# Performance work log

Hardware: AMD Instinct MI355X
Metric: run time of the kernel (lower is better)

Reference implementation:

```python
import jax, jax.numpy as jnp
import numpy as np

B, S, D = 2, 2048, 2048
H = 16
HD = D // H  # 128


def setup_inputs() -> dict:
    key = jax.random.key(0)
    k1, k2, k3 = jax.random.split(key, 3)
    scale = 0.02
    return {
        "hidden_states": jax.random.normal(k1, (B, S, D), dtype=jnp.float32),
        "c_attn_w": jax.random.normal(k2, (D, 3 * D), dtype=jnp.float32) * scale,
        "c_attn_b": jnp.zeros((3 * D,), dtype=jnp.float32),
        "c_proj_w": jax.random.normal(k3, (D, D), dtype=jnp.float32) * scale,
        "c_proj_b": jnp.zeros((D,), dtype=jnp.float32),
    }


def reference(hidden_states, c_attn_w, c_attn_b, c_proj_w, c_proj_b):
    # Conv1D: x @ W + b  (W is [in, out])
    qkv = hidden_states @ c_attn_w + c_attn_b            # [B,S,3D]
    q, k, v = jnp.split(qkv, 3, axis=-1)                 # each [B,S,D]

    def split_heads(t):
        return t.reshape(B, S, H, HD).transpose(0, 2, 1, 3)  # [B,H,S,HD]

    q, k, v = split_heads(q), split_heads(k), split_heads(v)

    # scaled dot-product scores (scale_attn_weights=True)
    scores = jnp.einsum("bhqd,bhkd->bhqk", q, k) / jnp.sqrt(
        jnp.asarray(HD, dtype=q.dtype)
    )
    # causal mask (tril bias buffer)
    causal = jnp.tril(jnp.ones((S, S), dtype=bool))
    mask_value = jnp.finfo(scores.dtype).min
    scores = jnp.where(causal[None, None, :, :], scores, mask_value)

    attn = jax.nn.softmax(scores, axis=-1)               # [B,H,S,S]
    ctx = jnp.einsum("bhqk,bhkd->bhqd", attn, v)         # [B,H,S,HD]
    ctx = ctx.transpose(0, 2, 1, 3).reshape(B, S, D)      # merge heads

    out = ctx @ c_proj_w + c_proj_b                       # [B,S,D]
    return out
```

## Files before the change

kernel.cpp:

```cpp
#include <hip/hip_runtime.h>

typedef unsigned short u16;
typedef __bf16 bfx8 __attribute__((ext_vector_type(8)));
typedef float f32x4 __attribute__((ext_vector_type(4)));

#define B_ 2
#define S_ 2048
#define D_ 2048
#define H_ 16
#define HD_ 128
#define SD_ 6144

__device__ __forceinline__ u16 f2bf(float f) {
  union { float f; unsigned u; } v; v.f = f;
  unsigned r = v.u + 0x7fffu + ((v.u >> 16) & 1u);
  return (u16)(r >> 16);
}
__device__ __forceinline__ float bf2f(u16 b) {
  union { unsigned u; float f; } v; v.u = ((unsigned)b) << 16;
  return v.f;
}
__device__ __forceinline__ void gload_lds16(const void* g, void* l) {
  __builtin_amdgcn_global_load_lds((const __attribute__((address_space(1))) void*)g,
                                   (__attribute__((address_space(3))) void*)l, 16, 0, 0);
}

#define BAR() do { asm volatile("" ::: "memory"); __builtin_amdgcn_s_barrier(); \
                   asm volatile("" ::: "memory"); } while (0)
#define WAIT_VM4() asm volatile("s_waitcnt vmcnt(4)" ::: "memory")
#define WAIT_VM3() asm volatile("s_waitcnt vmcnt(3)" ::: "memory")
#define WAIT_VM0() asm volatile("s_waitcnt vmcnt(0)" ::: "memory")

__device__ __forceinline__ void tile_coords(int BM, int BN, int& m0, int& n0) {
  int flat = blockIdx.x + gridDim.x * blockIdx.y;
  int xcd = flat & 7, li = flat >> 3;
  int MW = gridDim.y >> 3;
  int half = li >> 1, nn = li & 1;
  int mloc = half % MW, nw = half / MW;
  m0 = (xcd * MW + mloc) * BM;
  n0 = (nw * 2 + nn) * BN;
}

__global__ __launch_bounds__(256) void cvt_kernel(const float* __restrict__ in,
                                                  u16* __restrict__ out, int n4) {
  int i = blockIdx.x * blockDim.x + threadIdx.x;
  int stride = gridDim.x * blockDim.x;
  for (int idx = i; idx < n4; idx += stride) {
    float4 v = ((const float4*)in)[idx];
    uint2 o;
    o.x = (unsigned)f2bf(v.x) | ((unsigned)f2bf(v.y) << 16);
    o.y = (unsigned)f2bf(v.z) | ((unsigned)f2bf(v.w) << 16);
    ((uint2*)out)[idx] = o;
  }
}

__global__ __launch_bounds__(256) void transpose_cvt(const float* __restrict__ in,
                                                     u16* __restrict__ out,
                                                     int R, int C) {
  __shared__ float tile[32][33];
  int tx = threadIdx.x, ty = threadIdx.y;
  int c0 = blockIdx.x * 32, r0 = blockIdx.y * 32;
  for (int i = 0; i < 4; ++i)
    tile[ty + i * 8][tx] = in[(size_t)(r0 + ty + i * 8) * C + c0 + tx];
  __syncthreads();
  for (int i = 0; i < 4; ++i)
    out[(size_t)(c0 + ty + i * 8) * R + r0 + tx] = f2bf(tile[tx][ty + i * 8]);
}

__global__ __launch_bounds__(256) void transpose_v(const u16* __restrict__ qkv,
                                                   u16* __restrict__ vt) {
  __shared__ u16 tile[32][33];
  int tx = threadIdx.x, ty = threadIdx.y;
  int bh = blockIdx.z;
  int b = bh >> 4, h = bh & 15;
  int s0 = blockIdx.x * 32, d0 = blockIdx.y * 32;
  const u16* src = qkv + (size_t)b * S_ * SD_ + 2 * D_ + h * HD_;
  for (int i = 0; i < 4; ++i)
    tile[ty + i * 8][tx] = src[(size_t)(s0 + ty + i * 8) * SD_ + d0 + tx];
  __syncthreads();
  u16* dst = vt + (size_t)bh * HD_ * S_;
  for (int i = 0; i < 4; ++i)
    dst[(size_t)(d0 + ty + i * 8) * S_ + s0 + tx] = tile[tx][ty + i * 8];
}

template<int OUT_BF16>
__global__ __launch_bounds__(512, 2) void gemm8p(const u16* __restrict__ A,
                                                 const u16* __restrict__ Bt,
                                                 const float* __restrict__ bias,
                                                 void* __restrict__ Cout,
                                                 int M, int N, int K) {
  __shared__ u16 lds[2][2][2][256 * 32];

  int t = threadIdx.x, l = t & 63, w = t >> 6;
  int lr = l & 15, lg = l >> 4;
  int wr = w >> 2, wc = w & 3;

  int m0, n0;
  tile_coords(256, 256, m0, n0);

  f32x4 acc[8][4];
#pragma unroll
  for (int i = 0; i < 8; ++i)
#pragma unroll
    for (int j = 0; j < 4; ++j)
#pragma unroll
      for (int r = 0; r < 4; ++r) acc[i][j][r] = 0.0f;

  int srow = t >> 2, sc = t & 3;
  const u16* As0 = A  + (size_t)(m0 + srow) * K + ((sc ^ ((srow >> 1) & 3)) * 8);
  const u16* Bs0 = Bt + (size_t)(n0 + srow) * K + ((sc ^ ((srow >> 1) & 3)) * 8);
  size_t hstep = (size_t)128 * K;

#define STG_A(BUF, KH, KOFF) do { \
    gload_lds16(As0 + (KOFF),         &lds[0][BUF][KH][t * 8]); \
    gload_lds16(As0 + hstep + (KOFF), &lds[0][BUF][KH][4096 + t * 8]); \
  } while (0)
#define STG_B(BUF, KH, KOFF) do { \
    gload_lds16(Bs0 + (KOFF),         &lds[1][BUF][KH][t * 8]); \
    gload_lds16(Bs0 + hstep + (KOFF), &lds[1][BUF][KH][4096 + t * 8]); \
  } while (0)

  int NT = K >> 6;
  int rsw = (lg ^ ((lr >> 1) & 3)) * 8;
  int arow = wr * 128 + lr;
  int brow = wc * 64 + lr;

  STG_A(0, 0, 0); STG_B(0, 0, 0); STG_A(0, 1, 32); STG_B(0, 1, 32);
  WAIT_VM4();
  BAR();

  for (int g = 0; g < NT; ++g) {
    int cb = g & 1, sb = cb ^ 1;
    int koff = (g + 1) * 64;
    bool stg = (g + 1 < NT);
    bfx8 a0[4], a1[4], bfr[4];

    if (stg) { STG_A(sb, 0, koff); STG_B(sb, 0, koff); }
#pragma unroll
    for (int i = 0; i < 4; ++i) {
      a0[i] = *(const bfx8*)&lds[0][cb][0][(arow + i * 16) * 32 + rsw];
      a1[i] = *(const bfx8*)&lds[0][cb][0][(arow + 64 + i * 16) * 32 + rsw];
    }
#pragma unroll
    for (int j = 0; j < 4; ++j)
      bfr[j] = *(const bfx8*)&lds[1][cb][0][(brow + j * 16) * 32 + rsw];
    __builtin_amdgcn_s_setprio(1);
#pragma unroll
    for (int i = 0; i < 4; ++i)
#pragma unroll
      for (int j = 0; j < 4; ++j) {
        acc[i][j]     = __builtin_amdgcn_mfma_f32_16x16x32_bf16(a0[i], bfr[j], acc[i][j], 0, 0, 0);
        acc[4 + i][j] = __builtin_amdgcn_mfma_f32_16x16x32_bf16(a1[i], bfr[j], acc[4 + i][j], 0, 0, 0);
      }
    __builtin_amdgcn_s_setprio(0);
    if (stg) WAIT_VM4(); else WAIT_VM0();
    BAR();

    if (stg) { STG_A(sb, 1, koff + 32); STG_B(sb, 1, koff + 32); }
#pragma unroll
    for (int i = 0; i < 4; ++i) {
      a0[i] = *(const bfx8*)&lds[0][cb][1][(arow + i * 16) * 32 + rsw];
      a1[i] = *(const bfx8*)&lds[0][cb][1][(arow + 64 + i * 16) * 32 + rsw];
    }
#pragma unroll
    for (int j = 0; j < 4; ++j)
      bfr[j] = *(const bfx8*)&lds[1][cb][1][(brow + j * 16) * 32 + rsw];
    __builtin_amdgcn_s_setprio(1);
#pragma unroll
    for (int i = 0; i < 4; ++i)
#pragma unroll
      for (int j = 0; j < 4; ++j) {
        acc[i][j]     = __builtin_amdgcn_mfma_f32_16x16x32_bf16(a0[i], bfr[j], acc[i][j], 0, 0, 0);
        acc[4 + i][j] = __builtin_amdgcn_mfma_f32_16x16x32_bf16(a1[i], bfr[j], acc[4 + i][j], 0, 0, 0);
      }
    __builtin_amdgcn_s_setprio(0);
    if (stg) WAIT_VM4(); else WAIT_VM0();
    BAR();
  }
#undef STG_A
#undef STG_B

  for (int i = 0; i < 8; ++i) {
    int row = m0 + wr * 128 + i * 16 + lg * 4;
    for (int j = 0; j < 4; ++j) {
      int col = n0 + wc * 64 + j * 16 + lr;
      float bz = bias[col];
      for (int r = 0; r < 4; ++r) {
        float v = acc[i][j][r] + bz;
        if (OUT_BF16)
          ((u16*)Cout)[(size_t)(row + r) * N + col] = f2bf(v);
        else
          ((float*)Cout)[(size_t)(row + r) * N + col] = v;
      }
    }
  }
}

template<int OUT_BF16>
__global__ __launch_bounds__(512, 2) void gemm2p(const u16* __restrict__ A,
                                                 const u16* __restrict__ Bt,
                                                 const float* __restrict__ bias,
                                                 void* __restrict__ Cout,
                                                 int M, int N, int K) {
  __shared__ u16 ldsA[2][2][128 * 32];
  __shared__ u16 ldsB[2][2][256 * 32];

  int t = threadIdx.x, l = t & 63, w = t >> 6;
  int lr = l & 15, lg = l >> 4;
  int wr = w >> 2, wc = w & 3;

  int m0, n0;
  tile_coords(128, 256, m0, n0);

  f32x4 acc[4][4];
#pragma unroll
  for (int i = 0; i < 4; ++i)
#pragma unroll
    for (int j = 0; j < 4; ++j)
#pragma unroll
      for (int r = 0; r < 4; ++r) acc[i][j][r] = 0.0f;

  int srow = t >> 2, sc = t & 3;
  int csw = (sc ^ ((srow >> 1) & 3)) * 8;
  const u16* As0 = A  + (size_t)(m0 + srow) * K + csw;
  const u16* Bs0 = Bt + (size_t)(n0 + srow) * K + csw;
  size_t hstep = (size_t)128 * K;

#define STG_A(BUF, KH, KOFF) \
    gload_lds16(As0 + (KOFF), &ldsA[BUF][KH][t * 8])
#define STG_B(BUF, KH, KOFF) do { \
    gload_lds16(Bs0 + (KOFF),         &ldsB[BUF][KH][t * 8]); \
    gload_lds16(Bs0 + hstep + (KOFF), &ldsB[BUF][KH][4096 + t * 8]); \
  } while (0)

  int NT = K >> 6;
  int rsw = (lg ^ ((lr >> 1) & 3)) * 8;
  int arow = wr * 64 + lr;
  int brow = wc * 64 + lr;

  STG_A(0, 0, 0); STG_B(0, 0, 0); STG_A(0, 1, 32); STG_B(0, 1, 32);
  WAIT_VM3();
  BAR();

  for (int g = 0; g < NT; ++g) {
    int cb = g & 1, sb = cb ^ 1;
    int koff = (g + 1) * 64;
    bool stg = (g + 1 < NT);
    bfx8 af[4], bfr[4];

#pragma unroll
    for (int i = 0; i < 4; ++i)
      af[i] = *(const bfx8*)&ldsA[cb][0][(arow + i * 16) * 32 + rsw];
#pragma unroll
    for (int j = 0; j < 4; ++j)
      bfr[j] = *(const bfx8*)&ldsB[cb][0][(brow + j * 16) * 32 + rsw];
    if (stg) { STG_A(sb, 0, koff); STG_B(sb, 0, koff); }
    BAR();
    __builtin_amdgcn_s_setprio(1);
#pragma unroll
    for (int i = 0; i < 4; ++i)
#pragma unroll
      for (int j = 0; j < 4; ++j)
        acc[i][j] = __builtin_amdgcn_mfma_f32_16x16x32_bf16(af[i], bfr[j], acc[i][j], 0, 0, 0);
    __builtin_amdgcn_s_setprio(0);
    if (stg) WAIT_VM3(); else WAIT_VM0();
    BAR();

#pragma unroll
    for (int i = 0; i < 4; ++i)
      af[i] = *(const bfx8*)&ldsA[cb][1][(arow + i * 16) * 32 + rsw];
#pragma unroll
    for (int j = 0; j < 4; ++j)
      bfr[j] = *(const bfx8*)&ldsB[cb][1][(brow + j * 16) * 32 + rsw];
    if (stg) { STG_A(sb, 1, koff + 32); STG_B(sb, 1, koff + 32); }
    BAR();
    __builtin_amdgcn_s_setprio(1);
#pragma unroll
    for (int i = 0; i < 4; ++i)
#pragma unroll
      for (int j = 0; j < 4; ++j)
        acc[i][j] = __builtin_amdgcn_mfma_f32_16x16x32_bf16(af[i], bfr[j], acc[i][j], 0, 0, 0);
    __builtin_amdgcn_s_setprio(0);
    if (stg) WAIT_VM3();
    BAR();
  }
#undef STG_A
#undef STG_B

  for (int i = 0; i < 4; ++i) {
    int row = m0 + wr * 64 + i * 16 + lg * 4;
    for (int j = 0; j < 4; ++j) {
      int col = n0 + wc * 64 + j * 16 + lr;
      float bz = bias[col];
      for (int r = 0; r < 4; ++r) {
        float v = acc[i][j][r] + bz;
        if (OUT_BF16)
          ((u16*)Cout)[(size_t)(row + r) * N + col] = f2bf(v);
        else
          ((float*)Cout)[(size_t)(row + r) * N + col] = v;
      }
    }
  }
}

#define STAGE(BUF, KT) do {                                                        \
    int kc_ = ((t & 15) ^ ((t >> 4) & 7)) * 8;                                     \
    for (int i_ = 0; i_ < 4; ++i_)                                                 \
      gload_lds16(kbase + (size_t)((KT) * 64 + i_ * 16 + (t >> 4)) * SD_ + kc_,    \
                  &Klds[BUF][i_ * 2048 + t * 8]);                                  \
    int vc_ = (KT) * 64 + (((t & 7) ^ ((t >> 3) & 7)) * 8);                        \
    for (int i_ = 0; i_ < 4; ++i_)                                                 \
      gload_lds16(vbase + (size_t)(i_ * 32 + (t >> 3)) * S_ + vc_,                 \
                  &Vlds[BUF][i_ * 2048 + t * 8]);                                  \
  } while (0)

__global__ __launch_bounds__(256) void attn_kernel(const u16* __restrict__ qkv,
                                                   const u16* __restrict__ vt,
                                                   u16* __restrict__ ctx) {
  __shared__ u16 Klds[2][64 * 128];
  __shared__ u16 Vlds[2][128 * 64];
  __shared__ u16 Plds[4][16 * 64];

  int t = threadIdx.x, l = t & 63, w = t >> 6;
  int lr = l & 15, lg = l >> 4;
  int sw = lr & 7;
  int bid = blockIdx.x;
  int pr = bid >> 5, bh = bid & 31;
  int b = bh >> 4, h = bh & 15;
  const float scale = 0.08838834764831845f;

  const u16* kbase = qkv + (size_t)b * S_ * SD_ + D_ + h * HD_;
  const u16* vbase = vt + (size_t)bh * HD_ * S_;

  for (int sgi = 0; sgi < 2; ++sgi) {
    int qt = sgi ? pr : (31 - pr);
    int q0 = qt * 64;
    int wbase = q0 + w * 16;
    int nt = qt + 1;

    bfx8 qf[4];
    {
      const u16* qbase = qkv + (size_t)(b * S_ + wbase) * SD_ + h * HD_;
      for (int kk = 0; kk < 4; ++kk) {
        const u16* src = qbase + (size_t)lr * SD_ + kk * 32 + lg * 8;
        union { uint4 u; u16 s[8]; bfx8 bv; } iv, ov;
        iv.u = *(const uint4*)src;
        for (int j = 0; j < 8; ++j) ov.s[j] = f2bf(bf2f(iv.s[j]) * scale);
        qf[kk] = ov.bv;
      }
    }

    f32x4 o[8];
    float mrun = -INFINITY, lrun = 0.0f;
    for (int ht = 0; ht < 8; ++ht)
      for (int r = 0; r < 4; ++r) o[ht][r] = 0.0f;

    if (sgi) __syncthreads();
    STAGE(0, 0);

    for (int kt = 0; kt < nt; ++kt) {
      int cur = kt & 1;
      __syncthreads();
      if (kt + 1 < nt) STAGE(cur ^ 1, kt + 1);

      int kb0 = kt * 64;

      f32x4 sacc[4];
      for (int n = 0; n < 4; ++n)
        for (int r = 0; r < 4; ++r) sacc[n][r] = 0.0f;
      for (int n = 0; n < 4; ++n) {
        bfx8 kf[4];
        int krow = n * 16 + lr;
        for (int kk = 0; kk < 4; ++kk)
          kf[kk] = *(const bfx8*)&Klds[cur][krow * 128 + ((kk * 4 + lg) ^ sw) * 8];
        for (int kk = 0; kk < 4; ++kk)
          sacc[n] = __builtin_amdgcn_mfma_f32_16x16x32_bf16(kf[kk], qf[kk], sacc[n], 0, 0, 0);
      }

      int q = wbase + lr;
      if (kb0 + 63 > wbase) {
        for (int n = 0; n < 4; ++n)
          for (int r = 0; r < 4; ++r)
            if (kb0 + n * 16 + lg * 4 + r > q) sacc[n][r] = -INFINITY;
      }
      float tm = -INFINITY;
      for (int n = 0; n < 4; ++n) {
        float a = fmaxf(fmaxf(sacc[n][0], sacc[n][1]),
                        fmaxf(sacc[n][2], sacc[n][3]));
        tm = fmaxf(tm, a);
      }
      tm = fmaxf(tm, __shfl_xor(tm, 16, 64));
      tm = fmaxf(tm, __shfl_xor(tm, 32, 64));
      float mold = mrun;
      float mnew = fmaxf(mold, tm);
      if (__any((int)(mnew > mold))) {
        float corr = __expf(mold - mnew);
        lrun *= corr;
        mrun = mnew;
        for (int r = 0; r < 4; ++r) {
          float c = __shfl(corr, lg * 4 + r, 16);
          for (int ht = 0; ht < 8; ++ht) o[ht][r] *= c;
        }
      }
      float mm = mrun;
      float psum = 0.0f;
      for (int n = 0; n < 4; ++n) {
        float p0 = __expf(sacc[n][0] - mm);
        float p1 = __expf(sacc[n][1] - mm);
        float p2 = __expf(sacc[n][2] - mm);
        float p3 = __expf(sacc[n][3] - mm);
        psum += (p0 + p1) + (p2 + p3);
        uint2 pk;
        pk.x = (unsigned)f2bf(p0) | ((unsigned)f2bf(p1) << 16);
        pk.y = (unsigned)f2bf(p2) | ((unsigned)f2bf(p3) << 16);
        *(uint2*)&Plds[w][lr * 64 + ((n * 2 + (lg >> 1)) ^ sw) * 8 + (lg & 1) * 4] = pk;
      }
      psum += __shfl_xor(psum, 16, 64);
      psum += __shfl_xor(psum, 32, 64);
      lrun += psum;

      for (int kk = 0; kk < 2; ++kk) {
        bfx8 pa = *(const bfx8*)&Plds[w][lr * 64 + ((kk * 4 + lg) ^ sw) * 8];
        for (int ht = 0; ht < 8; ++ht) {
          bfx8 vb = *(const bfx8*)&Vlds[cur][(ht * 16 + lr) * 64 + ((kk * 4 + lg) ^ sw) * 8];
          o[ht] = __builtin_amdgcn_mfma_f32_16x16x32_bf16(pa, vb, o[ht], 0, 0, 0);
        }
      }
    }

    for (int r = 0; r < 4; ++r) {
      float inv = 1.0f / __shfl(lrun, lg * 4 + r, 16);
      int qa = wbase + lg * 4 + r;
      u16* dst = ctx + (size_t)(b * S_ + qa) * D_ + h * HD_;
      for (int ht = 0; ht < 8; ++ht)
        dst[ht * 16 + lr] = f2bf(o[ht][r] * inv);
    }
  }
}

extern "C" void kernel_launch(void* const* d_in, const int* in_sizes, int n_in,
                              void* d_out, int out_size, void* d_ws, size_t ws_size,
                              hipStream_t stream) {
  const float* hs     = (const float*)d_in[0];
  const float* w_attn = (const float*)d_in[1];
  const float* b_attn = (const float*)d_in[2];
  const float* w_proj = (const float*)d_in[3];
  const float* b_proj = (const float*)d_in[4];

  u16* Xb     = (u16*)d_ws;
  u16* Wqkvt  = Xb     + 8388608;
  u16* Wprojt = Wqkvt  + 12582912;
  u16* qkvb   = Wprojt + 4194304;
  u16* Vt     = qkvb   + 25165824;
  u16* ctxb   = Vt     + 8388608;

  cvt_kernel<<<2048, 256, 0, stream>>>(hs, Xb, (B_ * S_ * D_) / 4);
  transpose_cvt<<<dim3(192, 64), dim3(32, 8), 0, stream>>>(w_attn, Wqkvt, D_, 3 * D_);
  transpose_cvt<<<dim3(64, 64), dim3(32, 8), 0, stream>>>(w_proj, Wprojt, D_, D_);
  gemm8p<1><<<dim3(24, 16), 512, 0, stream>>>(Xb, Wqkvt, b_attn, qkvb, 4096, 6144, 2048);
  transpose_v<<<dim3(64, 4, 32), dim3(32, 8), 0, stream>>>(qkvb, Vt);
  attn_kernel<<<dim3(512), 256, 0, stream>>>(qkvb, Vt, ctxb);
  gemm2p<0><<<dim3(8, 32), 512, 0, stream>>>(ctxb, Wprojt, b_proj, d_out, 4096, 2048, 2048);
}
```

Baseline: 269.8 us.

## Process 32 query rows per wave in attention to reuse K/V fragments

Each attention block now uses 2 waves instead of 4, and each wave handles two 16-row query subtiles. K and V fragments read from LDS are reused across both subtiles, and the staging loops are split into 8 iterations to fit the smaller thread count. This halves the LDS reads of K and V per MFMA and gives each wave more independent MFMAs to interleave. The cost is higher register pressure and fewer waves per block, which can reduce latency hiding.

```diff
diff --git a/kernel.cpp b/kernel.cpp
--- a/kernel.cpp
+++ b/kernel.cpp
@@ -305,21 +305,21 @@
 
 #define STAGE(BUF, KT) do {                                                        \
     int kc_ = ((t & 15) ^ ((t >> 4) & 7)) * 8;                                     \
-    for (int i_ = 0; i_ < 4; ++i_)                                                 \
-      gload_lds16(kbase + (size_t)((KT) * 64 + i_ * 16 + (t >> 4)) * SD_ + kc_,    \
-                  &Klds[BUF][i_ * 2048 + t * 8]);                                  \
+    for (int i_ = 0; i_ < 8; ++i_)                                                 \
+      gload_lds16(kbase + (size_t)((KT) * 64 + i_ * 8 + (t >> 4)) * SD_ + kc_,     \
+                  &Klds[BUF][i_ * 1024 + t * 8]);                                  \
     int vc_ = (KT) * 64 + (((t & 7) ^ ((t >> 3) & 7)) * 8);                        \
-    for (int i_ = 0; i_ < 4; ++i_)                                                 \
-      gload_lds16(vbase + (size_t)(i_ * 32 + (t >> 3)) * S_ + vc_,                 \
-                  &Vlds[BUF][i_ * 2048 + t * 8]);                                  \
+    for (int i_ = 0; i_ < 8; ++i_)                                                 \
+      gload_lds16(vbase + (size_t)(i_ * 16 + (t >> 3)) * S_ + vc_,                 \
+                  &Vlds[BUF][i_ * 1024 + t * 8]);                                  \
   } while (0)
 
-__global__ __launch_bounds__(256) void attn_kernel(const u16* __restrict__ qkv,
+__global__ __launch_bounds__(128) void attn_kernel(const u16* __restrict__ qkv,
                                                    const u16* __restrict__ vt,
                                                    u16* __restrict__ ctx) {
   __shared__ u16 Klds[2][64 * 128];
   __shared__ u16 Vlds[2][128 * 64];
-  __shared__ u16 Plds[4][16 * 64];
+  __shared__ u16 Plds[2][32 * 64];
 
   int t = threadIdx.x, l = t & 63, w = t >> 6;
   int lr = l & 15, lg = l >> 4;
@@ -335,25 +335,28 @@
   for (int sgi = 0; sgi < 2; ++sgi) {
     int qt = sgi ? pr : (31 - pr);
     int q0 = qt * 64;
-    int wbase = q0 + w * 16;
+    int wbase = q0 + w * 32;
     int nt = qt + 1;
 
-    bfx8 qf[4];
-    {
-      const u16* qbase = qkv + (size_t)(b * S_ + wbase) * SD_ + h * HD_;
+    bfx8 qf[2][4];
+    for (int m = 0; m < 2; ++m) {
+      const u16* qbase = qkv + (size_t)(b * S_ + wbase + m * 16) * SD_ + h * HD_;
       for (int kk = 0; kk < 4; ++kk) {
         const u16* src = qbase + (size_t)lr * SD_ + kk * 32 + lg * 8;
         union { uint4 u; u16 s[8]; bfx8 bv; } iv, ov;
         iv.u = *(const uint4*)src;
         for (int j = 0; j < 8; ++j) ov.s[j] = f2bf(bf2f(iv.s[j]) * scale);
-        qf[kk] = ov.bv;
-      }
-    }
-
-    f32x4 o[8];
-    float mrun = -INFINITY, lrun = 0.0f;
-    for (int ht = 0; ht < 8; ++ht)
-      for (int r = 0; r < 4; ++r) o[ht][r] = 0.0f;
+        qf[m][kk] = ov.bv;
+      }
+    }
+
+    f32x4 o[2][8];
+    float mrun[2], lrun[2];
+    for (int m = 0; m < 2; ++m) {
+      for (int ht = 0; ht < 8; ++ht)
+        for (int r = 0; r < 4; ++r) o[m][ht][r] = 0.0f;
+      mrun[m] = -INFINITY; lrun[m] = 0.0f;
+    }
 
     if (sgi) __syncthreads();
     STAGE(0, 0);
@@ -365,76 +368,85 @@
 
       int kb0 = kt * 64;
 
-      f32x4 sacc[4];
-      for (int n = 0; n < 4; ++n)
-        for (int r = 0; r < 4; ++r) sacc[n][r] = 0.0f;
+      f32x4 sacc[2][4];
+      for (int m = 0; m < 2; ++m)
+        for (int n = 0; n < 4; ++n)
+          for (int r = 0; r < 4; ++r) sacc[m][n][r] = 0.0f;
       for (int n = 0; n < 4; ++n) {
         bfx8 kf[4];
         int krow = n * 16 + lr;
         for (int kk = 0; kk < 4; ++kk)
           kf[kk] = *(const bfx8*)&Klds[cur][krow * 128 + ((kk * 4 + lg) ^ sw) * 8];
-        for (int kk = 0; kk < 4; ++kk)
-          sacc[n] = __builtin_amdgcn_mfma_f32_16x16x32_bf16(kf[kk], qf[kk], sacc[n], 0, 0, 0);
-      }
-
-      int q = wbase + lr;
-      if (kb0 + 63 > wbase) {
-        for (int n = 0; n < 4; ++n)
-          for (int r = 0; r < 4; ++r)
-            if (kb0 + n * 16 + lg * 4 + r > q) sacc[n][r] = -INFINITY;
-      }
-      float tm = -INFINITY;
-      for (int n = 0; n < 4; ++n) {
-        float a = fmaxf(fmaxf(sacc[n][0], sacc[n][1]),
-                        fmaxf(sacc[n][2], sacc[n][3]));
-        tm = fmaxf(tm, a);
-      }
-      tm = fmaxf(tm, __shfl_xor(tm, 16, 64));
-      tm = fmaxf(tm, __shfl_xor(tm, 32, 64));
-      float mold = mrun;
-      float mnew = fmaxf(mold, tm);
-      if (__any((int)(mnew > mold))) {
-        float corr = __expf(mold - mnew);
-        lrun *= corr;
-        mrun = mnew;
-        for (int r = 0; r < 4; ++r) {
-          float c = __shfl(corr, lg * 4 + r, 16);
-          for (int ht = 0; ht < 8; ++ht) o[ht][r] *= c;
+        for (int m = 0; m < 2; ++m)
+          for (int kk = 0; kk < 4; ++kk)
+            sacc[m][n] = __builtin_amdgcn_mfma_f32_16x16x32_bf16(kf[kk], qf[m][kk], sacc[m][n], 0, 0, 0);
+      }
+
+      for (int m = 0; m < 2; ++m) {
+        int base = wbase + m * 16;
+        int q = base + lr;
+        int row = m * 16 + lr;
+        if (kb0 + 63 > base) {
+          for (int n = 0; n < 4; ++n)
+            for (int r = 0; r < 4; ++r)
+              if (kb0 + n * 16 + lg * 4 + r > q) sacc[m][n][r] = -INFINITY;
         }
-      }
-      float mm = mrun;
-      float psum = 0.0f;
-      for (int n = 0; n < 4; ++n) {
-        float p0 = __expf(sacc[n][0] - mm);
-        float p1 = __expf(sacc[n][1] - mm);
-        float p2 = __expf(sacc[n][2] - mm);
-        float p3 = __expf(sacc[n][3] - mm);
-        psum += (p0 + p1) + (p2 + p3);
-        uint2 pk;
-        pk.x = (unsigned)f2bf(p0) | ((unsigned)f2bf(p1) << 16);
-        pk.y = (unsigned)f2bf(p2) | ((unsigned)f2bf(p3) << 16);
-        *(uint2*)&Plds[w][lr * 64 + ((n * 2 + (lg >> 1)) ^ sw) * 8 + (lg & 1) * 4] = pk;
-      }
-      psum += __shfl_xor(psum, 16, 64);
-      psum += __shfl_xor(psum, 32, 64);
-      lrun += psum;
+        float tm = -INFINITY;
+        for (int n = 0; n < 4; ++n) {
+          float a = fmaxf(fmaxf(sacc[m][n][0], sacc[m][n][1]),
+                          fmaxf(sacc[m][n][2], sacc[m][n][3]));
+          tm = fmaxf(tm, a);
+        }
+        tm = fmaxf(tm, __shfl_xor(tm, 16, 64));
+        tm = fmaxf(tm, __shfl_xor(tm, 32, 64));
+        float mold = mrun[m];
+        float mnew = fmaxf(mold, tm);
+        if (__any((int)(mnew > mold))) {
+          float corr = __expf(mold - mnew);
+          lrun[m] *= corr;
+          mrun[m] = mnew;
+          for (int r = 0; r < 4; ++r) {
+            float c = __shfl(corr, lg * 4 + r, 16);
+            for (int ht = 0; ht < 8; ++ht) o[m][ht][r] *= c;
+          }
+        }
+        float mm = mrun[m];
+        float psum = 0.0f;
+        for (int n = 0; n < 4; ++n) {
+          float p0 = __expf(sacc[m][n][0] - mm);
+          float p1 = __expf(sacc[m][n][1] - mm);
+          float p2 = __expf(sacc[m][n][2] - mm);
+          float p3 = __expf(sacc[m][n][3] - mm);
+          psum += (p0 + p1) + (p2 + p3);
+          uint2 pk;
+          pk.x = (unsigned)f2bf(p0) | ((unsigned)f2bf(p1) << 16);
+          pk.y = (unsigned)f2bf(p2) | ((unsigned)f2bf(p3) << 16);
+          *(uint2*)&Plds[w][row * 64 + ((n * 2 + (lg >> 1)) ^ sw) * 8 + (lg & 1) * 4] = pk;
+        }
+        psum += __shfl_xor(psum, 16, 64);
+        psum += __shfl_xor(psum, 32, 64);
+        lrun[m] += psum;
+      }
 
       for (int kk = 0; kk < 2; ++kk) {
-        bfx8 pa = *(const bfx8*)&Plds[w][lr * 64 + ((kk * 4 + lg) ^ sw) * 8];
+        bfx8 pa0 = *(const bfx8*)&Plds[w][lr * 64 + ((kk * 4 + lg) ^ sw) * 8];
+        bfx8 pa1 = *(const bfx8*)&Plds[w][(16 + lr) * 64 + ((kk * 4 + lg) ^ sw) * 8];
         for (int ht = 0; ht < 8; ++ht) {
           bfx8 vb = *(const bfx8*)&Vlds[cur][(ht * 16 + lr) * 64 + ((kk * 4 + lg) ^ sw) * 8];
-          o[ht] = __builtin_amdgcn_mfma_f32_16x16x32_bf16(pa, vb, o[ht], 0, 0, 0);
+          o[0][ht] = __builtin_amdgcn_mfma_f32_16x16x32_bf16(pa0, vb, o[0][ht], 0, 0, 0);
+          o[1][ht] = __builtin_amdgcn_mfma_f32_16x16x32_bf16(pa1, vb, o[1][ht], 0, 0, 0);
         }
       }
     }
 
-    for (int r = 0; r < 4; ++r) {
-      float inv = 1.0f / __shfl(lrun, lg * 4 + r, 16);
-      int qa = wbase + lg * 4 + r;
-      u16* dst = ctx + (size_t)(b * S_ + qa) * D_ + h * HD_;
-      for (int ht = 0; ht < 8; ++ht)
-        dst[ht * 16 + lr] = f2bf(o[ht][r] * inv);
-    }
+    for (int m = 0; m < 2; ++m)
+      for (int r = 0; r < 4; ++r) {
+        float inv = 1.0f / __shfl(lrun[m], lg * 4 + r, 16);
+        int qa = wbase + m * 16 + lg * 4 + r;
+        u16* dst = ctx + (size_t)(b * S_ + qa) * D_ + h * HD_;
+        for (int ht = 0; ht < 8; ++ht)
+          dst[ht * 16 + lr] = f2bf(o[m][ht][r] * inv);
+      }
   }
 }
 
@@ -459,6 +471,6 @@
   transpose_cvt<<<dim3(64, 64), dim3(32, 8), 0, stream>>>(w_proj, Wprojt, D_, D_);
   gemm8p<1><<<dim3(24, 16), 512, 0, stream>>>(Xb, Wqkvt, b_attn, qkvb, 4096, 6144, 2048);
   transpose_v<<<dim3(64, 4, 32), dim3(32, 8), 0, stream>>>(qkvb, Vt);
-  attn_kernel<<<dim3(512), 256, 0, stream>>>(qkvb, Vt, ctxb);
+  attn_kernel<<<dim3(512), 128, 0, stream>>>(qkvb, Vt, ctxb);
   gemm2p<0><<<dim3(8, 32), 512, 0, stream>>>(ctxb, Wprojt, b_proj, d_out, 4096, 2048, 2048);
 }
```

Measured after the change: 290.8 us. +7.8%, slower.
